# Kernel tuning notes

Hardware: AMD Instinct MI355X
Metric: run time of the kernel (lower is better)

The kernel has to match this reference:

```python
import jax, jax.numpy as jnp
import numpy as np

B, N, DIM = 2, 2048, 1024
H, DH = 16, 64
INNER = H * DH  # 1024
SCALE = DH ** -0.5
EPS = 1e-5


def setup_inputs() -> dict:
    key = jax.random.key(0)
    ks = jax.random.split(key, 7)
    s = 0.02
    return {
        "x": jax.random.normal(ks[0], (B, N, DIM), dtype=jnp.float32),
        "ln_gamma": jnp.ones((DIM,), jnp.float32),
        "ln_beta": jnp.zeros((DIM,), jnp.float32),
        "W_qkv": jax.random.normal(ks[1], (DIM, 3 * INNER), jnp.float32) * s,
        "b_qkv": jnp.zeros((3 * INNER,), jnp.float32),
        "W_out": jax.random.normal(ks[2], (INNER, DIM), jnp.float32) * s,
        "b_out": jnp.zeros((DIM,), jnp.float32),
    }


def reference(x, ln_gamma, ln_beta, W_qkv, b_qkv, W_out, b_out):
    # LayerNorm over last dim
    mu = jnp.mean(x, axis=-1, keepdims=True)
    var = jnp.mean(jnp.square(x - mu), axis=-1, keepdims=True)
    xn = (x - mu) * jax.lax.rsqrt(var + EPS) * ln_gamma + ln_beta
    # QKV projection
    qkv = xn @ W_qkv + b_qkv                      # [b, n, 3*inner]
    q, k, v = jnp.split(qkv, 3, axis=-1)
    # [b, n, (h d)] -> [b, h, n, d]
    to_heads = lambda t: t.reshape(B, N, H, DH).transpose(0, 2, 1, 3)
    q, k, v = to_heads(q), to_heads(k), to_heads(v)
    # naive attention (explicit score matrix, matching the original)
    qk = jnp.einsum('bhnd,bhmd->bhnm', q, k) * SCALE
    attn = jax.nn.softmax(qk, axis=-1)
    out = jnp.einsum('bhnm,bhmd->bhnd', attn, v)  # [b, h, n, d]
    out = out.transpose(0, 2, 1, 3).reshape(B, N, INNER)
    return out @ W_out + b_out
```

## Files before the change

### kernel.cpp

```cpp
#include <hip/hip_runtime.h>

typedef unsigned short u16;
typedef unsigned int   u32;
typedef __attribute__((ext_vector_type(2)))  unsigned u32x2;
typedef __attribute__((ext_vector_type(4)))  float  f32x4;
typedef __attribute__((ext_vector_type(8)))  short  s16x8;

__device__ __forceinline__ u16 f2bf(float f) {
  unsigned u = __builtin_bit_cast(unsigned, f);
  u += 0x7FFFu + ((u >> 16) & 1u);
  return (u16)(u >> 16);
}

__device__ __forceinline__ float exp2g(float x) { return __builtin_amdgcn_exp2f(x); }

__device__ __forceinline__ void gload16(const void* g, void* l) {
  __builtin_amdgcn_global_load_lds(
      (const __attribute__((address_space(1))) void*)g,
      (__attribute__((address_space(3))) void*)l, 16, 0, 0);
}

__global__ __launch_bounds__(256) void ln_kernel(
    const float* __restrict__ x, const float* __restrict__ gamma,
    const float* __restrict__ beta, u16* __restrict__ xn)
{
  const int row = blockIdx.x, tid = threadIdx.x;
  const float* xr = x + (size_t)row * 1024;
  float4 v = *(const float4*)(xr + tid * 4);
  float s  = v.x + v.y + v.z + v.w;
  float s2 = v.x*v.x + v.y*v.y + v.z*v.z + v.w*v.w;
#pragma unroll
  for (int off = 32; off >= 1; off >>= 1) {
    s  += __shfl_xor(s,  off);
    s2 += __shfl_xor(s2, off);
  }
  __shared__ float red[8];
  const int w = tid >> 6, l = tid & 63;
  if (l == 0) { red[w] = s; red[w + 4] = s2; }
  __syncthreads();
  s  = red[0] + red[1] + red[2] + red[3];
  s2 = red[4] + red[5] + red[6] + red[7];
  const float mu  = s * (1.0f / 1024.0f);
  const float var = s2 * (1.0f / 1024.0f) - mu * mu;
  const float rs  = rsqrtf(var + 1e-5f);
  float4 g  = *(const float4*)(gamma + tid * 4);
  float4 be = *(const float4*)(beta  + tid * 4);
  ushort4 o;
  o.x = f2bf((v.x - mu) * rs * g.x + be.x);
  o.y = f2bf((v.y - mu) * rs * g.y + be.y);
  o.z = f2bf((v.z - mu) * rs * g.z + be.z);
  o.w = f2bf((v.w - mu) * rs * g.w + be.w);
  *(ushort4*)(xn + (size_t)row * 1024 + tid * 4) = o;
}

__global__ void transpose_cvt(const float* __restrict__ in, u16* __restrict__ out,
                              int R, int C)
{
  __shared__ float t[32][33];
  const int bc = blockIdx.x * 32, br = blockIdx.y * 32;
  const int x = threadIdx.x;
#pragma unroll
  for (int i = threadIdx.y; i < 32; i += 8)
    t[i][x] = in[(size_t)(br + i) * C + bc + x];
  __syncthreads();
#pragma unroll
  for (int i = threadIdx.y; i < 32; i += 8)
    out[(size_t)(bc + i) * R + br + x] = f2bf(t[x][i]);
}

__device__ __forceinline__ void store_out(float* p, float v) { *p = v; }
__device__ __forceinline__ void store_out(u16* p, float v)   { *p = f2bf(v); }

template <typename OutT>
__global__ __launch_bounds__(256) void gemm_bt(
    const u16* __restrict__ A, const u16* __restrict__ Bt,
    const float* __restrict__ bias, OutT* __restrict__ C,
    int M, int N, int K)
{
  __shared__ u16 As[2][128 * 32];
  __shared__ u16 Bs[2][128 * 32];
  const int tid = threadIdx.x;
  const int w = tid >> 6, l = tid & 63;
  const int g = l >> 4, li = l & 15;
  const int bm = blockIdx.y * 128, bn = blockIdx.x * 128;
  const int wr = (w >> 1) * 64, wc = (w & 1) * 64;

  f32x4 acc[4][4] = {};

  const int ar0 = tid >> 2,          as0 = tid & 3;
  const int ar1 = (tid + 256) >> 2,  as1 = (tid + 256) & 3;
  const u16* pa0 = A  + (size_t)(bm + ar0) * K + 8 * (as0 ^ (ar0 & 3));
  const u16* pa1 = A  + (size_t)(bm + ar1) * K + 8 * (as1 ^ (ar1 & 3));
  const u16* pb0 = Bt + (size_t)(bn + ar0) * K + 8 * (as0 ^ (ar0 & 3));
  const u16* pb1 = Bt + (size_t)(bn + ar1) * K + 8 * (as1 ^ (ar1 & 3));

  auto stage = [&](int b, int kt) {
    gload16(pa0 + kt, &As[b][w * 512]);
    gload16(pa1 + kt, &As[b][2048 + w * 512]);
    gload16(pb0 + kt, &Bs[b][w * 512]);
    gload16(pb1 + kt, &Bs[b][2048 + w * 512]);
  };

  stage(0, 0);

  int buf = 0;
  for (int kt = 0; kt < K; kt += 32) {
    __syncthreads();
    if (kt + 32 < K) stage(buf ^ 1, kt + 32);

    const u16* as = &As[buf][0];
    const u16* bs = &Bs[buf][0];

    s16x8 af[4], bf[4];
#pragma unroll
    for (int m = 0; m < 4; ++m) {
      const int row = wr + m * 16 + li;
      af[m] = *(const s16x8*)(as + row * 32 + 8 * (g ^ (row & 3)));
    }
#pragma unroll
    for (int n = 0; n < 4; ++n) {
      const int row = wc + n * 16 + li;
      bf[n] = *(const s16x8*)(bs + row * 32 + 8 * (g ^ (row & 3)));
    }
    __builtin_amdgcn_s_setprio(1);
#pragma unroll
    for (int m = 0; m < 4; ++m)
#pragma unroll
      for (int n = 0; n < 4; ++n)
        acc[m][n] = __builtin_amdgcn_mfma_f32_16x16x32_bf16(af[m], bf[n], acc[m][n], 0, 0, 0);
    __builtin_amdgcn_s_setprio(0);

    buf ^= 1;
  }

#pragma unroll
  for (int n = 0; n < 4; ++n) {
    const int col = bn + wc + n * 16 + li;
    const float bv = bias[col];
#pragma unroll
    for (int m = 0; m < 4; ++m) {
      const int row0 = bm + wr + m * 16 + g * 4;
#pragma unroll
      for (int r = 0; r < 4; ++r)
        store_out(C + (size_t)(row0 + r) * N + col, acc[m][n][r] + bv);
    }
  }
}

__global__ __launch_bounds__(256, 4) void attn_kernel(
    const u16* __restrict__ qkv, u16* __restrict__ outp)
{
  __shared__ u16 Ks[2][4096];
  __shared__ u16 Vt[4096];
  __shared__ u16 Pl[4 * 1024];

  const int tid = threadIdx.x;
  const int w = tid >> 6, l = tid & 63;
  const int g = l >> 4, li = l & 15;

  const int lb = (blockIdx.x & 7) * 128 + (blockIdx.x >> 3);
  const int qt = lb & 31;
  const int h  = (lb >> 5) & 15;
  const int bb = lb >> 9;
  const size_t baserow = (size_t)bb * 2048;

  const int qbase = qt * 64 + w * 16;
  const u16* qp = qkv + (baserow + qbase + li) * 3072 + h * 64 + 8 * g;
  const s16x8 qf0 = *(const s16x8*)(qp);
  const s16x8 qf1 = *(const s16x8*)(qp + 32);

  const int kr0 = tid >> 3,         kc0 = tid & 7;
  const int kr1 = (tid + 256) >> 3, kc1 = (tid + 256) & 7;
  const u16* kg0 = qkv + (baserow + kr0) * 3072 + 1024 + h * 64 + 8 * (kc0 ^ (kr0 & 7));
  const u16* kg1 = qkv + (baserow + kr1) * 3072 + 1024 + h * 64 + 8 * (kc1 ^ (kr1 & 7));

  const int vp = tid >> 3, dg = tid & 7;
  const u16* vgA = qkv + (baserow + 2 * vp)     * 3072 + 2048 + h * 64 + 8 * dg;
  const u16* vgB = qkv + (baserow + 2 * vp + 1) * 3072 + 2048 + h * 64 + 8 * dg;

  auto issueK = [&](int b, int t) {
    const size_t koff = (size_t)t * (64 * 3072);
    gload16(kg0 + koff, &Ks[b][w * 512]);
    gload16(kg1 + koff, &Ks[b][2048 + w * 512]);
  };

  const float C1  = 0.18033688f;
  const float THR = 11.5416f;
  float M = -1e30f;
  f32x4 o[4] = {}, os = {};

  s16x8 ones;
#pragma unroll
  for (int j = 0; j < 8; ++j) ones[j] = (short)0x3F80;

  char* Pw = (char*)(Pl + w * 1024);
  const int pswz = (li & 7) << 4;

  issueK(0, 0);
  s16x8 va = *(const s16x8*)vgA;
  s16x8 vb = *(const s16x8*)vgB;

  int buf = 0;
  for (int t = 0; t < 32; ++t) {
#pragma unroll
    for (int j = 0; j < 8; ++j) {
      const int d = 8 * dg + j;
      const u32 val = (u32)(u16)va[j] | ((u32)(u16)vb[j] << 16);
      *(u32*)((char*)Vt + d * 128 + ((4 * vp) ^ ((((d ^ (d >> 3)) & 7)) << 4))) = val;
    }
    __syncthreads();

    if (t < 31) {
      issueK(buf ^ 1, t + 1);
      const size_t koff = (size_t)(t + 1) * (64 * 3072);
      va = *(const s16x8*)(vgA + koff);
      vb = *(const s16x8*)(vgB + koff);
    }

    const u16* kb = &Ks[buf][0];

    f32x4 s[4] = {};
    __builtin_amdgcn_s_setprio(1);
#pragma unroll
    for (int nk = 0; nk < 4; ++nk) {
      const int kvr = nk * 16 + li;
      const s16x8 kf0 = *(const s16x8*)((const char*)kb + kvr * 128 + 16 * ((0 + g) ^ (kvr & 7)));
      const s16x8 kf1 = *(const s16x8*)((const char*)kb + kvr * 128 + 16 * ((4 + g) ^ (kvr & 7)));
      s[nk] = __builtin_amdgcn_mfma_f32_16x16x32_bf16(kf0, qf0, s[nk], 0, 0, 0);
      s[nk] = __builtin_amdgcn_mfma_f32_16x16x32_bf16(kf1, qf1, s[nk], 0, 0, 0);
    }
    __builtin_amdgcn_s_setprio(0);

    float lm = fmaxf(fmaxf(s[0][0], s[0][1]), fmaxf(s[0][2], s[0][3]));
#pragma unroll
    for (int nk = 1; nk < 4; ++nk)
      lm = fmaxf(lm, fmaxf(fmaxf(s[nk][0], s[nk][1]), fmaxf(s[nk][2], s[nk][3])));
    lm = fmaxf(lm, __shfl_xor(lm, 16));
    lm = fmaxf(lm, __shfl_xor(lm, 32));
    lm *= C1;

    if (__any(lm > M + THR)) {
      const float mn = fmaxf(M, lm);
      const float a = exp2g(M - mn);
      M = mn;
      os[0] *= a;
#pragma unroll
      for (int nd = 0; nd < 4; ++nd)
#pragma unroll
        for (int r = 0; r < 4; ++r) o[nd][r] *= a;
    }

#pragma unroll
    for (int nk = 0; nk < 4; ++nk)
#pragma unroll
      for (int r = 0; r < 4; ++r)
        s[nk][r] = exp2g(fmaf(s[nk][r], C1, -M));

#pragma unroll
    for (int nk = 0; nk < 4; ++nk) {
      u32 lo, hi;
      asm("v_cvt_pk_bf16_f32 %0, %1, %2" : "=v"(lo) : "v"(s[nk][0]), "v"(s[nk][1]));
      asm("v_cvt_pk_bf16_f32 %0, %1, %2" : "=v"(hi) : "v"(s[nk][2]), "v"(s[nk][3]));
      *(u32x2*)(Pw + li * 128 + ((nk * 32 + 8 * g) ^ pswz)) = (u32x2){lo, hi};
    }
    asm volatile("s_waitcnt lgkmcnt(0)" ::: "memory");

    __builtin_amdgcn_s_setprio(1);
#pragma unroll
    for (int ks = 0; ks < 2; ++ks) {
      const s16x8 pf = *(const s16x8*)(Pw + li * 128 + ((ks * 64 + 16 * g) ^ pswz));
#pragma unroll
      for (int nd = 0; nd < 4; ++nd) {
        const int d = nd * 16 + li;
        const s16x8 vf = *(const s16x8*)((char*)Vt + d * 128 + ((ks * 64 + 16 * g) ^ (((d ^ (d >> 3)) & 7) << 4)));
        o[nd] = __builtin_amdgcn_mfma_f32_16x16x32_bf16(vf, pf, o[nd], 0, 0, 0);
      }
      os = __builtin_amdgcn_mfma_f32_16x16x32_bf16(ones, pf, os, 0, 0, 0);
    }
    __builtin_amdgcn_s_setprio(0);

    __syncthreads();
    buf ^= 1;
  }

  const float inv = 1.0f / os[0];
  const size_t row = baserow + qbase + li;
#pragma unroll
  for (int nd = 0; nd < 4; ++nd) {
    ushort4 st;
    st.x = f2bf(o[nd][0] * inv);
    st.y = f2bf(o[nd][1] * inv);
    st.z = f2bf(o[nd][2] * inv);
    st.w = f2bf(o[nd][3] * inv);
    *(ushort4*)(outp + row * 1024 + h * 64 + nd * 16 + 4 * g) = st;
  }
}

extern "C" void kernel_launch(void* const* d_in, const int* in_sizes, int n_in,
                              void* d_out, int out_size, void* d_ws, size_t ws_size,
                              hipStream_t stream)
{
  const float* x     = (const float*)d_in[0];
  const float* gamma = (const float*)d_in[1];
  const float* beta  = (const float*)d_in[2];
  const float* Wqkv  = (const float*)d_in[3];
  const float* bqkv  = (const float*)d_in[4];
  const float* Wout  = (const float*)d_in[5];
  const float* bout  = (const float*)d_in[6];
  float* out = (float*)d_out;

  char* ws = (char*)d_ws;
  u16* xn     = (u16*)(ws);
  u16* wqkv_t = (u16*)(ws + ((size_t)8  << 20));
  u16* wout_t = (u16*)(ws + ((size_t)14 << 20));
  u16* qkv    = (u16*)(ws + ((size_t)16 << 20));
  u16* attn   = (u16*)(ws + ((size_t)40 << 20));

  ln_kernel<<<4096, 256, 0, stream>>>(x, gamma, beta, xn);
  transpose_cvt<<<dim3(96, 32), dim3(32, 8), 0, stream>>>(Wqkv, wqkv_t, 1024, 3072);
  transpose_cvt<<<dim3(32, 32), dim3(32, 8), 0, stream>>>(Wout, wout_t, 1024, 1024);
  gemm_bt<u16><<<dim3(24, 32), 256, 0, stream>>>(xn, wqkv_t, bqkv, qkv, 4096, 3072, 1024);
  attn_kernel<<<1024, 256, 0, stream>>>(qkv, attn);
  gemm_bt<float><<<dim3(8, 32), 256, 0, stream>>>(attn, wout_t, bout, out, 4096, 1024, 1024);
}
```

Before: 135.7 us.

## Use 256x256-tile GEMM with XCD-aware block remap for QKV projection

```diff
diff --git a/kernel.cpp b/kernel.cpp
--- a/kernel.cpp
+++ b/kernel.cpp
@@ -68,6 +68,106 @@
     out[(size_t)(bc + i) * R + br + x] = f2bf(t[x][i]);
 }
 
+__global__ __launch_bounds__(512, 2) void gemm256_bt(
+    const u16* __restrict__ A, const u16* __restrict__ Bt,
+    const float* __restrict__ bias, u16* __restrict__ C,
+    int M, int N, int K, int NBX)
+{
+  __shared__ u16 As[2][16384];
+  __shared__ u16 Bs[2][16384];
+
+  const int tid = threadIdx.x;
+  const int w = tid >> 6, l = tid & 63;
+  const int g = l >> 4, li = l & 15;
+
+  const int nwg = NBX * ((M + 255) >> 8);
+  const int cpx = nwg >> 3;
+  const int lb  = (blockIdx.x & 7) * cpx + (blockIdx.x >> 3);
+  const int bn  = (lb % NBX) * 256;
+  const int bm  = (lb / NBX) * 256;
+
+  const int wr = (w >> 2) * 128, wc = (w & 3) * 64;
+
+  f32x4 acc[8][4] = {};
+
+  const u16* pa[4]; const u16* pb[4];
+#pragma unroll
+  for (int i = 0; i < 4; ++i) {
+    const int c = i * 512 + tid, row = c >> 3, slot = c & 7;
+    pa[i] = A  + (size_t)(bm + row) * K + 8 * (slot ^ (row & 7));
+    pb[i] = Bt + (size_t)(bn + row) * K + 8 * (slot ^ (row & 7));
+  }
+
+  auto stage = [&](int nb, int kt) {
+#pragma unroll
+    for (int i = 0; i < 4; ++i) {
+      u16* da = &As[nb][(i * 512 + w * 64) * 8];
+      u16* db = &Bs[nb][(i * 512 + w * 64) * 8];
+      gload16(pa[i] + kt, da);
+      gload16(pb[i] + kt, db);
+    }
+  };
+
+  stage(0, 0);
+  __syncthreads();
+
+  int buf = 0;
+  const int NT = K >> 6;
+  for (int t = 0; t < NT; ++t) {
+    if (t + 1 < NT) stage(buf ^ 1, (t + 1) << 6);
+
+    const u16* as = &As[buf][0];
+    const u16* bs = &Bs[buf][0];
+
+    s16x8 bf[4][2];
+#pragma unroll
+    for (int n = 0; n < 4; ++n)
+#pragma unroll
+      for (int kd = 0; kd < 2; ++kd) {
+        const int row = wc + n * 16 + li;
+        bf[n][kd] = *(const s16x8*)(bs + row * 64 + 8 * ((4 * kd + g) ^ (row & 7)));
+      }
+
+#pragma unroll
+    for (int mq = 0; mq < 4; ++mq) {
+      s16x8 af[2][2];
+#pragma unroll
+      for (int m2 = 0; m2 < 2; ++m2)
+#pragma unroll
+        for (int kd = 0; kd < 2; ++kd) {
+          const int row = wr + mq * 32 + m2 * 16 + li;
+          af[m2][kd] = *(const s16x8*)(as + row * 64 + 8 * ((4 * kd + g) ^ (row & 7)));
+        }
+      __builtin_amdgcn_s_setprio(1);
+#pragma unroll
+      for (int m2 = 0; m2 < 2; ++m2)
+#pragma unroll
+        for (int n = 0; n < 4; ++n)
+#pragma unroll
+          for (int kd = 0; kd < 2; ++kd)
+            acc[mq * 2 + m2][n] = __builtin_amdgcn_mfma_f32_16x16x32_bf16(
+                af[m2][kd], bf[n][kd], acc[mq * 2 + m2][n], 0, 0, 0);
+      __builtin_amdgcn_s_setprio(0);
+    }
+
+    __syncthreads();
+    buf ^= 1;
+  }
+
+#pragma unroll
+  for (int n = 0; n < 4; ++n) {
+    const int col = bn + wc + n * 16 + li;
+    const float bv = bias[col];
+#pragma unroll
+    for (int m = 0; m < 8; ++m) {
+      const int row0 = bm + wr + m * 16 + g * 4;
+#pragma unroll
+      for (int r = 0; r < 4; ++r)
+        C[(size_t)(row0 + r) * N + col] = f2bf(acc[m][n][r] + bv);
+    }
+  }
+}
+
 __device__ __forceinline__ void store_out(float* p, float v) { *p = v; }
 __device__ __forceinline__ void store_out(u16* p, float v)   { *p = f2bf(v); }
 
@@ -319,7 +419,7 @@
   ln_kernel<<<4096, 256, 0, stream>>>(x, gamma, beta, xn);
   transpose_cvt<<<dim3(96, 32), dim3(32, 8), 0, stream>>>(Wqkv, wqkv_t, 1024, 3072);
   transpose_cvt<<<dim3(32, 32), dim3(32, 8), 0, stream>>>(Wout, wout_t, 1024, 1024);
-  gemm_bt<u16><<<dim3(24, 32), 256, 0, stream>>>(xn, wqkv_t, bqkv, qkv, 4096, 3072, 1024);
+  gemm256_bt<<<192, 512, 0, stream>>>(xn, wqkv_t, bqkv, qkv, 4096, 3072, 1024, 12);
   attn_kernel<<<1024, 256, 0, stream>>>(qkv, attn);
   gemm_bt<float><<<dim3(8, 32), 256, 0, stream>>>(attn, wout_t, bout, out, 4096, 1024, 1024);
 }
```

New measurement: 141.8 us. 4.5% more time.
